# Performance work log

Hardware: AMD Instinct MI355X
Metric: run time of the kernel (lower is better)

The kernel has to match this reference:

```python
import jax, jax.numpy as jnp
import numpy as np

C = 1024
RANK = 8


def _layernorm(x, g, b, eps=1e-5):
    mu = jnp.mean(x, axis=-1, keepdims=True)
    var = jnp.var(x, axis=-1, keepdims=True)
    return (x - mu) * jax.lax.rsqrt(var + eps) * g + b


def setup_inputs() -> dict:
    key = jax.random.key(0)
    ks = jax.random.split(key, 10)
    B, T = 4, 4096
    x = jax.random.normal(ks[0], (B, T, C), dtype=jnp.float32)
    # parameters (match torch inits)
    W0 = jnp.eye(C, dtype=jnp.float32) * 0.1
    A_init = jax.random.normal(ks[1], (C, RANK), dtype=jnp.float32) * 0.01
    B_init = jnp.zeros((RANK, C), dtype=jnp.float32)
    log_lr = jnp.full((C,), float(np.log(0.1)), dtype=jnp.float32)
    s = 1.0 / np.sqrt(C)
    Wq = jax.random.uniform(ks[2], (C, C), minval=-s, maxval=s, dtype=jnp.float32)
    Wk = jax.random.uniform(ks[3], (C, C), minval=-s, maxval=s, dtype=jnp.float32)
    Wv = jax.random.uniform(ks[4], (C, C), minval=-s, maxval=s, dtype=jnp.float32)
    Wo = jax.random.uniform(ks[5], (C, C), minval=-s, maxval=s, dtype=jnp.float32)
    Wg = jax.random.uniform(ks[6], (C, C), minval=-s, maxval=s, dtype=jnp.float32)
    ln_g = jnp.ones((C,), dtype=jnp.float32)
    ln_b = jnp.zeros((C,), dtype=jnp.float32)
    ls_g = jnp.full((C,), 1e-4, dtype=jnp.float32)  # LayerScale gamma
    return {"x": x, "W0": W0, "A_init": A_init, "B_init": B_init,
            "log_lr": log_lr, "Wq": Wq, "Wk": Wk, "Wv": Wv, "Wo": Wo,
            "Wg": Wg, "ln_g": ln_g, "ln_b": ln_b, "ls_g": ls_g}


def reference(x, W0, A_init, B_init, log_lr, Wq, Wk, Wv, Wo, Wg, ln_g, ln_b, ls_g):
    B, T, _ = x.shape
    h = _layernorm(x, ln_g, ln_b)
    # dual-form TTT (training path: q/k/v projections, full K @ W0)
    Q = jnp.einsum('btc,dc->btd', h, Wq)
    K = jnp.einsum('btc,dc->btd', h, Wk)
    V = jnp.einsum('btc,dc->btd', h, Wv)
    lr = jnp.minimum(jnp.exp(log_lr), 1.0)  # clamp(max=1.0)
    y0 = jnp.einsum('btc,cd->btd', K, W0) + jnp.einsum('btr,rd->btd', jnp.einsum('btc,cr->btr', K, A_init), B_init)
    error = y0 - V
    loss = jnp.mean(error ** 2)
    gradient = K * error                     # [B,T,C]
    grad_cumsum = jnp.cumsum(gradient, axis=1)
    grad_shift = jnp.concatenate([jnp.zeros((B, 1, gradient.shape[-1]), gradient.dtype), grad_cumsum[:, :-1, :]], axis=1)
    correction = Q * lr[None, None, :] * grad_shift
    pos = jnp.arange(1, T + 1, dtype=correction.dtype)
    pos_scale = (1.0 / (1.0 + 0.1 * jnp.log(pos)))[None, :, None]
    out = y0 - correction * pos_scale
    # gate, out projection, layer scale, residual
    gate = jax.nn.sigmoid(jnp.einsum('btc,dc->btd', x, Wg))
    out = out * gate
    out = jnp.einsum('btc,dc->btd', out, Wo) * ls_g
    return (x + out, loss)
```

## Files before the change

kernel.cpp:

```cpp
#include <hip/hip_runtime.h>
#include <stdint.h>
#include <math.h>

typedef unsigned short u16;
typedef __attribute__((ext_vector_type(8))) short short8;
typedef __attribute__((ext_vector_type(4))) float f32x4;

__device__ __forceinline__ float bf2f(u16 u){
  union { unsigned int i; float f; } v; v.i = ((unsigned int)u) << 16; return v.f;
}
__device__ __forceinline__ u16 f2bf(float f){
  union { float f; unsigned int i; } v; v.f = f;
  return (u16)((v.i + 0x7FFFu + ((v.i >> 16) & 1u)) >> 16);
}

__global__ void ln_prep(const float* __restrict__ x, const float* __restrict__ g,
                        const float* __restrict__ bta, u16* __restrict__ h,
                        u16* __restrict__ xb, float* __restrict__ loss){
  if (blockIdx.x == 0 && threadIdx.x == 0) loss[0] = 0.f;
  int row = blockIdx.x, tid = threadIdx.x;
  const float4* xr = (const float4*)(x + (size_t)row * 1024);
  float4 v = xr[tid];
  float s  = v.x + v.y + v.z + v.w;
  float s2 = v.x*v.x + v.y*v.y + v.z*v.z + v.w*v.w;
  #pragma unroll
  for (int o = 32; o > 0; o >>= 1){ s += __shfl_down(s, o); s2 += __shfl_down(s2, o); }
  __shared__ float red[8];
  if ((tid & 63) == 0){ red[tid >> 6] = s; red[4 + (tid >> 6)] = s2; }
  __syncthreads();
  float ts = red[0]+red[1]+red[2]+red[3];
  float t2 = red[4]+red[5]+red[6]+red[7];
  float mu   = ts * (1.0f/1024.0f);
  float var  = t2 * (1.0f/1024.0f) - mu*mu;
  float rstd = rsqrtf(var + 1e-5f);
  float4 gg = ((const float4*)g)[tid];
  float4 bb = ((const float4*)bta)[tid];
  ushort4 hv, xv;
  hv.x = f2bf((v.x-mu)*rstd*gg.x + bb.x);
  hv.y = f2bf((v.y-mu)*rstd*gg.y + bb.y);
  hv.z = f2bf((v.z-mu)*rstd*gg.z + bb.z);
  hv.w = f2bf((v.w-mu)*rstd*gg.w + bb.w);
  xv.x = f2bf(v.x); xv.y = f2bf(v.y); xv.z = f2bf(v.z); xv.w = f2bf(v.w);
  ((ushort4*)h )[(size_t)row*256 + tid] = hv;
  ((ushort4*)xb)[(size_t)row*256 + tid] = xv;
}

__global__ void conv5(const float* __restrict__ a, const float* __restrict__ b,
                      const float* __restrict__ c, const float* __restrict__ d,
                      const float* __restrict__ e,
                      u16* oa, u16* ob, u16* oc, u16* od, u16* oe){
  int sel = blockIdx.y;
  const float* s = sel==0?a : sel==1?b : sel==2?c : sel==3?d : e;
  u16* o = sel==0?oa : sel==1?ob : sel==2?oc : sel==3?od : oe;
  int i = blockIdx.x*256 + threadIdx.x;
  float4 v = ((const float4*)s)[i];
  ushort4 r; r.x=f2bf(v.x); r.y=f2bf(v.y); r.z=f2bf(v.z); r.w=f2bf(v.w);
  ((ushort4*)o)[i] = r;
}

__global__ void weff_k(const float* __restrict__ W0, const float* __restrict__ Ai,
                       const float* __restrict__ Bi, u16* __restrict__ Wet){
  __shared__ float tile[32][33];
  int d0 = blockIdx.x*32, e0 = blockIdx.y*32;
  int tid = threadIdx.x;
  int lr = tid >> 5, lc = tid & 31;
  #pragma unroll
  for (int s = 0; s < 4; ++s){
    int e = e0 + s*8 + lr, d = d0 + lc;
    float v = W0[(size_t)e*1024 + d];
    #pragma unroll
    for (int r = 0; r < 8; ++r) v += Ai[e*8 + r] * Bi[(size_t)r*1024 + d];
    tile[s*8 + lr][lc] = v;
  }
  __syncthreads();
  #pragma unroll
  for (int s = 0; s < 4; ++s){
    int d = d0 + s*8 + lr, e = e0 + lc;
    Wet[(size_t)d*1024 + e] = f2bf(tile[lc][s*8 + lr]);
  }
}

#define VMW(N)  asm volatile("s_waitcnt vmcnt(" #N ")" ::: "memory")
#define LGKM0   asm volatile("s_waitcnt lgkmcnt(0)" ::: "memory")
#define SBAR    __builtin_amdgcn_s_barrier()
#define SCHED0  __builtin_amdgcn_sched_barrier(0)

template<int EPI>
__device__ __forceinline__ void gemm256_body(const u16* __restrict__ A, const u16* __restrict__ Bm,
    u16* __restrict__ Cb, float* __restrict__ Cf, const float* __restrict__ lsg,
    const float* __restrict__ xres, int mblk, int nblk)
{
  __shared__ u16 As[4][8192];
  __shared__ u16 Bs[4][8192];
  const int tid  = threadIdx.x;
  const int lane = tid & 63;
  const int w    = tid >> 6;
  const int wm = w >> 2, wn = w & 3;
  const int l15 = lane & 15, quad = lane >> 4;
  const int m0 = mblk * 256, n0 = nblk * 256;

  const int sl   = (lane & 7) ^ (lane >> 3);
  const int srow = 2*(w*8 + (lane >> 3)) + (sl >> 2);
  const int scol = (sl & 3) * 8;
  const u16* gA = A  + (size_t)(m0 + srow)*1024 + scol;
  const u16* gB = Bm + (size_t)(n0 + srow)*1024 + scol;
  const int ldsOff = w * 512;

  const int phys8 = (((((l15 & 1) << 2) | quad) ^ (l15 >> 1))) * 8;
  const int rdA = (wm*64 + (l15 >> 1))*64 + phys8;
  const int rdB = (wn*32 + (l15 >> 1))*64 + phys8;

  f32x4 acc[8][4] = {};

#define SA(T) do{ const int _ss=(T)&3; const size_t _k=(size_t)(T)*32; \
    __builtin_amdgcn_global_load_lds((const __attribute__((address_space(1))) unsigned int*)(gA + _k), \
        (__attribute__((address_space(3))) unsigned int*)(&As[_ss][ldsOff]), 16, 0, 0); \
    __builtin_amdgcn_global_load_lds((const __attribute__((address_space(1))) unsigned int*)(gA + _k + 131072), \
        (__attribute__((address_space(3))) unsigned int*)(&As[_ss][ldsOff + 4096]), 16, 0, 0); \
  }while(0)
#define SB(T) do{ const int _ss=(T)&3; const size_t _k=(size_t)(T)*32; \
    __builtin_amdgcn_global_load_lds((const __attribute__((address_space(1))) unsigned int*)(gB + _k), \
        (__attribute__((address_space(3))) unsigned int*)(&Bs[_ss][ldsOff]), 16, 0, 0); \
    __builtin_amdgcn_global_load_lds((const __attribute__((address_space(1))) unsigned int*)(gB + _k + 131072), \
        (__attribute__((address_space(3))) unsigned int*)(&Bs[_ss][ldsOff + 4096]), 16, 0, 0); \
  }while(0)

#define SLICE(T, DS, VMOP) do{ \
    const int _s = (T) & 3; \
    const u16* _as = &As[_s][0]; \
    const u16* _bs = &Bs[_s][0]; \
    short8 afv[8], bfv[4]; \
    bfv[0] = *(const short8*)(_bs + rdB); \
    bfv[1] = *(const short8*)(_bs + rdB + 512); \
    _Pragma("unroll") \
    for (int _i = 0; _i < 8; ++_i) afv[_i] = *(const short8*)(_as + rdA + _i*512); \
    if (DS) SA((T)+3); \
    SBAR; LGKM0; SCHED0; \
    __builtin_amdgcn_s_setprio(1); \
    _Pragma("unroll") \
    for (int _i = 0; _i < 8; ++_i){ \
      acc[_i][0] = __builtin_amdgcn_mfma_f32_16x16x32_bf16(afv[_i], bfv[0], acc[_i][0], 0, 0, 0); \
      acc[_i][1] = __builtin_amdgcn_mfma_f32_16x16x32_bf16(afv[_i], bfv[1], acc[_i][1], 0, 0, 0); \
    } \
    __builtin_amdgcn_s_setprio(0); SCHED0; SBAR; \
    bfv[2] = *(const short8*)(_bs + rdB + 1024); \
    bfv[3] = *(const short8*)(_bs + rdB + 1536); \
    if (DS) SB((T)+3); \
    VMOP; \
    SBAR; LGKM0; SCHED0; \
    __builtin_amdgcn_s_setprio(1); \
    _Pragma("unroll") \
    for (int _i = 0; _i < 8; ++_i){ \
      acc[_i][2] = __builtin_amdgcn_mfma_f32_16x16x32_bf16(afv[_i], bfv[2], acc[_i][2], 0, 0, 0); \
      acc[_i][3] = __builtin_amdgcn_mfma_f32_16x16x32_bf16(afv[_i], bfv[3], acc[_i][3], 0, 0, 0); \
    } \
    __builtin_amdgcn_s_setprio(0); SCHED0; SBAR; \
  }while(0)

  SA(0); SB(0); SA(1); SB(1); SA(2); SB(2);
  VMW(8);
  SBAR;

  #pragma unroll 1
  for (int t = 0; t < 28; t += 4){
    SLICE(t+0, 1, VMW(8));
    SLICE(t+1, 1, VMW(8));
    SLICE(t+2, 1, VMW(8));
    SLICE(t+3, 1, VMW(8));
  }
  SLICE(28, 1, VMW(8));
  SLICE(29, 0, VMW(4));
  SLICE(30, 0, VMW(0));
  SLICE(31, 0, (void)0);
#undef SLICE
#undef SA
#undef SB

  const int rbase = quad * 4;
  if (EPI == 0){
    #pragma unroll
    for (int i = 0; i < 8; ++i){
      int row = m0 + wm*128 + i*16 + rbase;
      #pragma unroll
      for (int j = 0; j < 4; ++j){
        int col = n0 + wn*64 + j*16 + l15;
        #pragma unroll
        for (int r = 0; r < 4; ++r)
          Cb[(size_t)(row + r)*1024 + col] = f2bf(acc[i][j][r]);
      }
    }
  } else {
    float lsv[4];
    #pragma unroll
    for (int j = 0; j < 4; ++j) lsv[j] = lsg[n0 + wn*64 + j*16 + l15];
    #pragma unroll
    for (int i = 0; i < 8; ++i){
      int row = m0 + wm*128 + i*16 + rbase;
      #pragma unroll
      for (int j = 0; j < 4; ++j){
        int col = n0 + wn*64 + j*16 + l15;
        #pragma unroll
        for (int r = 0; r < 4; ++r){
          size_t idx = (size_t)(row + r)*1024 + col;
          Cf[idx] = acc[i][j][r] * lsv[j] + xres[idx];
        }
      }
    }
  }
}

__global__ __launch_bounds__(512, 2) void gemm_qkvg(
    const u16* __restrict__ h, const u16* __restrict__ xb,
    const u16* __restrict__ Wqb, const u16* __restrict__ Wkb,
    const u16* __restrict__ Wvb, const u16* __restrict__ Wgb,
    u16* __restrict__ Qb, u16* __restrict__ Kb,
    u16* __restrict__ Vb, u16* __restrict__ Gb){
  int bid = blockIdx.x;
  int swz = (bid & 7) * 128 + (bid >> 3);
  int mblk = swz >> 4;
  int rem  = swz & 15;
  int sel  = rem >> 2, nblk = rem & 3;
  const u16* A  = (sel == 3) ? xb : h;
  const u16* Bm = sel==0?Wqb : sel==1?Wkb : sel==2?Wvb : Wgb;
  u16* Out      = sel==0?Qb  : sel==1?Kb  : sel==2?Vb  : Gb;
  gemm256_body<0>(A, Bm, Out, nullptr, nullptr, nullptr, mblk, nblk);
}

__global__ __launch_bounds__(512, 2) void gemm_plain(
    const u16* __restrict__ A, const u16* __restrict__ Bm, u16* __restrict__ C){
  int bid = blockIdx.x;
  int swz = (bid & 7) * 32 + (bid >> 3);
  gemm256_body<0>(A, Bm, C, nullptr, nullptr, nullptr, swz >> 2, swz & 3);
}

__global__ __launch_bounds__(512, 2) void gemm_final(
    const u16* __restrict__ A, const u16* __restrict__ Bm,
    float* __restrict__ C, const float* __restrict__ lsg,
    const float* __restrict__ xres){
  int bid = blockIdx.x;
  int swz = (bid & 7) * 32 + (bid >> 3);
  gemm256_body<1>(A, Bm, nullptr, C, lsg, xres, swz >> 2, swz & 3);
}

__global__ void scan1(const u16* __restrict__ Kb, const u16* __restrict__ Vb,
                      const u16* __restrict__ Yb, float* __restrict__ part,
                      float* __restrict__ loss){
  int tid = threadIdx.x;
  int c = blockIdx.x*256 + tid;
  int ch = blockIdx.y, b = blockIdx.z;
  size_t base = ((size_t)b*4096 + (size_t)ch*128)*1024 + c;
  float g = 0.f, ls = 0.f;
  #pragma unroll 8
  for (int t = 0; t < 128; ++t){
    size_t idx = base + (size_t)t*1024;
    float kv = bf2f(Kb[idx]), vv = bf2f(Vb[idx]), yv = bf2f(Yb[idx]);
    float e = yv - vv;
    g += kv*e; ls += e*e;
  }
  part[((size_t)(b*32 + ch))*1024 + c] = g;
  #pragma unroll
  for (int o = 32; o > 0; o >>= 1) ls += __shfl_down(ls, o);
  __shared__ float red[4];
  if ((tid & 63) == 0) red[tid >> 6] = ls;
  __syncthreads();
  if (tid == 0) atomicAdd(loss, red[0]+red[1]+red[2]+red[3]);
}

__global__ void scan2(const u16* __restrict__ Kb, const u16* __restrict__ Vb,
                      const u16* __restrict__ Yb, const u16* __restrict__ Qb,
                      const u16* __restrict__ Gb, const float* __restrict__ part,
                      const float* __restrict__ llr, u16* __restrict__ OutPre){
  int tid = threadIdx.x;
  int c = blockIdx.x*256 + tid;
  int ch = blockIdx.y, b = blockIdx.z;
  float run = 0.f;
  for (int j = 0; j < ch; ++j) run += part[((size_t)(b*32 + j))*1024 + c];
  float lrc = fminf(expf(llr[c]), 1.0f);
  size_t base = ((size_t)b*4096 + (size_t)ch*128)*1024 + c;
  #pragma unroll 4
  for (int t = 0; t < 128; ++t){
    size_t idx = base + (size_t)t*1024;
    float kv = bf2f(Kb[idx]), vv = bf2f(Vb[idx]), yv = bf2f(Yb[idx]);
    float qv = bf2f(Qb[idx]), gl = bf2f(Gb[idx]);
    float e = yv - vv;
    int tg = ch*128 + t + 1;
    float ps = 1.0f/(1.0f + 0.1f*logf((float)tg));
    float gate = 1.0f/(1.0f + expf(-gl));
    float o = (yv - qv*lrc*run*ps) * gate;
    OutPre[idx] = f2bf(o);
    run += kv*e;
  }
}

__global__ void finloss(const float* __restrict__ loss, float* __restrict__ o){
  o[0] = loss[0] * (1.0f/16777216.0f);
}

extern "C" void kernel_launch(void* const* d_in, const int* in_sizes, int n_in,
                              void* d_out, int out_size, void* d_ws, size_t ws_size,
                              hipStream_t stream){
  const float* x   = (const float*)d_in[0];
  const float* W0  = (const float*)d_in[1];
  const float* Ai  = (const float*)d_in[2];
  const float* Bi  = (const float*)d_in[3];
  const float* llr = (const float*)d_in[4];
  const float* Wq  = (const float*)d_in[5];
  const float* Wk  = (const float*)d_in[6];
  const float* Wv  = (const float*)d_in[7];
  const float* Wo  = (const float*)d_in[8];
  const float* Wg  = (const float*)d_in[9];
  const float* lng = (const float*)d_in[10];
  const float* lnb = (const float*)d_in[11];
  const float* lsg = (const float*)d_in[12];
  float* out = (float*)d_out;

  const size_t TOK = 16384, CC = 1024;
  char* p = (char*)d_ws;
  float* loss = (float*)p; p += 256;
  u16* h   = (u16*)p; p += TOK*CC*2;
  u16* xb  = (u16*)p; p += TOK*CC*2;
  u16* Qb  = (u16*)p; p += TOK*CC*2;
  u16* Kb  = (u16*)p; p += TOK*CC*2;
  u16* Vb  = (u16*)p; p += TOK*CC*2;
  u16* Gb  = (u16*)p; p += TOK*CC*2;
  u16* Wqb = (u16*)p; p += CC*CC*2;
  u16* Wkb = (u16*)p; p += CC*CC*2;
  u16* Wvb = (u16*)p; p += CC*CC*2;
  u16* Wgb = (u16*)p; p += CC*CC*2;
  u16* Wob = (u16*)p; p += CC*CC*2;
  u16* Wet = (u16*)p; p += CC*CC*2;
  float* part = (float*)p; p += (size_t)4*32*1024*4;

  ln_prep<<<16384, 256, 0, stream>>>(x, lng, lnb, h, xb, loss);
  conv5<<<dim3(1024, 5), 256, 0, stream>>>(Wq, Wk, Wv, Wg, Wo, Wqb, Wkb, Wvb, Wgb, Wob);
  weff_k<<<dim3(32, 32), 256, 0, stream>>>(W0, Ai, Bi, Wet);
  gemm_qkvg<<<1024, 512, 0, stream>>>(h, xb, Wqb, Wkb, Wvb, Wgb, Qb, Kb, Vb, Gb);
  gemm_plain<<<256, 512, 0, stream>>>(Kb, Wet, h);
  scan1<<<dim3(4, 32, 4), 256, 0, stream>>>(Kb, Vb, h, part, loss);
  scan2<<<dim3(4, 32, 4), 256, 0, stream>>>(Kb, Vb, h, Qb, Gb, part, llr, Qb);
  gemm_final<<<256, 512, 0, stream>>>(Qb, Wob, out, lsg, x);
  finloss<<<1, 1, 0, stream>>>(loss, out + 16777216);
}
```

Before: 458.1 us.

## Restructure GEMM k-slice pipeline to one barrier per slice with hoisted prefetch

Each k-slice now waits on vmcnt, does a single barrier, issues both A and B global-to-LDS prefetches for slice T+3, then loads all LDS fragments and runs all 32 MFMAs in one block. Before, each slice was split into two halves with four barriers, explicit lgkmcnt waits and setprio toggling. The aim is to cut barrier and sync overhead and let the compiler interleave LDS reads with MFMAs. The risks are less deliberate wave scheduling, more registers held live for B fragments, and a possible race from prefetching into the 4-deep ring while other waves may still be reading slot T-1.

```diff
diff --git a/kernel.cpp b/kernel.cpp
--- a/kernel.cpp
+++ b/kernel.cpp
@@ -81,7 +81,6 @@
 }
 
 #define VMW(N)  asm volatile("s_waitcnt vmcnt(" #N ")" ::: "memory")
-#define LGKM0   asm volatile("s_waitcnt lgkmcnt(0)" ::: "memory")
 #define SBAR    __builtin_amdgcn_s_barrier()
 #define SCHED0  __builtin_amdgcn_sched_barrier(0)
 
@@ -125,53 +124,39 @@
         (__attribute__((address_space(3))) unsigned int*)(&Bs[_ss][ldsOff + 4096]), 16, 0, 0); \
   }while(0)
 
-#define SLICE(T, DS, VMOP) do{ \
+#define SLICE(T, VMOP, DS) do{ \
+    VMOP; \
+    SCHED0; SBAR; SCHED0; \
+    if (DS){ SA((T)+3); SB((T)+3); } \
     const int _s = (T) & 3; \
     const u16* _as = &As[_s][0]; \
     const u16* _bs = &Bs[_s][0]; \
     short8 afv[8], bfv[4]; \
-    bfv[0] = *(const short8*)(_bs + rdB); \
-    bfv[1] = *(const short8*)(_bs + rdB + 512); \
+    _Pragma("unroll") \
+    for (int _j = 0; _j < 4; ++_j) bfv[_j] = *(const short8*)(_bs + rdB + _j*512); \
     _Pragma("unroll") \
     for (int _i = 0; _i < 8; ++_i) afv[_i] = *(const short8*)(_as + rdA + _i*512); \
-    if (DS) SA((T)+3); \
-    SBAR; LGKM0; SCHED0; \
-    __builtin_amdgcn_s_setprio(1); \
     _Pragma("unroll") \
     for (int _i = 0; _i < 8; ++_i){ \
-      acc[_i][0] = __builtin_amdgcn_mfma_f32_16x16x32_bf16(afv[_i], bfv[0], acc[_i][0], 0, 0, 0); \
-      acc[_i][1] = __builtin_amdgcn_mfma_f32_16x16x32_bf16(afv[_i], bfv[1], acc[_i][1], 0, 0, 0); \
+      _Pragma("unroll") \
+      for (int _j = 0; _j < 4; ++_j) \
+        acc[_i][_j] = __builtin_amdgcn_mfma_f32_16x16x32_bf16(afv[_i], bfv[_j], acc[_i][_j], 0, 0, 0); \
     } \
-    __builtin_amdgcn_s_setprio(0); SCHED0; SBAR; \
-    bfv[2] = *(const short8*)(_bs + rdB + 1024); \
-    bfv[3] = *(const short8*)(_bs + rdB + 1536); \
-    if (DS) SB((T)+3); \
-    VMOP; \
-    SBAR; LGKM0; SCHED0; \
-    __builtin_amdgcn_s_setprio(1); \
-    _Pragma("unroll") \
-    for (int _i = 0; _i < 8; ++_i){ \
-      acc[_i][2] = __builtin_amdgcn_mfma_f32_16x16x32_bf16(afv[_i], bfv[2], acc[_i][2], 0, 0, 0); \
-      acc[_i][3] = __builtin_amdgcn_mfma_f32_16x16x32_bf16(afv[_i], bfv[3], acc[_i][3], 0, 0, 0); \
-    } \
-    __builtin_amdgcn_s_setprio(0); SCHED0; SBAR; \
   }while(0)
 
   SA(0); SB(0); SA(1); SB(1); SA(2); SB(2);
-  VMW(8);
-  SBAR;
 
   #pragma unroll 1
   for (int t = 0; t < 28; t += 4){
-    SLICE(t+0, 1, VMW(8));
-    SLICE(t+1, 1, VMW(8));
-    SLICE(t+2, 1, VMW(8));
-    SLICE(t+3, 1, VMW(8));
-  }
-  SLICE(28, 1, VMW(8));
-  SLICE(29, 0, VMW(4));
-  SLICE(30, 0, VMW(0));
-  SLICE(31, 0, (void)0);
+    SLICE(t+0, VMW(8), 1);
+    SLICE(t+1, VMW(8), 1);
+    SLICE(t+2, VMW(8), 1);
+    SLICE(t+3, VMW(8), 1);
+  }
+  SLICE(28, VMW(8), 1);
+  SLICE(29, VMW(8), 0);
+  SLICE(30, VMW(4), 0);
+  SLICE(31, VMW(0), 0);
 #undef SLICE
 #undef SA
 #undef SB
```

Result: faster. 430.7 us (-6.0%).
